# Kernel tuning notes

Measured on AMD Instinct MI355X. Metric: run time of the kernel, lower is better.

The kernel has to match this reference:

```python
import jax, jax.numpy as jnp
import numpy as np

B, L, E, H = 2, 2048, 1024, 16
HD = E // H  # 64
THETA = 10000.0


def setup_inputs() -> dict:
    key = jax.random.key(0)
    ks = jax.random.split(key, 9)
    s = 1.0 / np.sqrt(E)
    return {
        "x": jax.random.normal(ks[0], (B, L, E), jnp.float32),
        "Wq": jax.random.normal(ks[1], (E, E), jnp.float32) * s,
        "bq": jax.random.normal(ks[2], (E,), jnp.float32) * 0.01,
        "Wk": jax.random.normal(ks[3], (E, E), jnp.float32) * s,
        "bk": jax.random.normal(ks[4], (E,), jnp.float32) * 0.01,
        "Wv": jax.random.normal(ks[5], (E, E), jnp.float32) * s,
        "bv": jax.random.normal(ks[6], (E,), jnp.float32) * 0.01,
        "Wo": jax.random.normal(ks[7], (E, E), jnp.float32) * s,
        "bo": jax.random.normal(ks[8], (E,), jnp.float32) * 0.01,
    }


def _rope_tables(seq_len, dim, dtype):
    # lucidrains RotaryEmbedding: inv_freq over even indices, each freq repeated twice (interleaved)
    inv_freq = 1.0 / (THETA ** (jnp.arange(0, dim, 2, dtype=jnp.float32) / dim))
    freqs = jnp.arange(seq_len, dtype=jnp.float32)[:, None] * inv_freq[None, :]  # [L, dim/2]
    freqs = jnp.repeat(freqs, 2, axis=-1)  # [L, dim] -> f0,f0,f1,f1,...
    return jnp.cos(freqs).astype(dtype), jnp.sin(freqs).astype(dtype)


def _rotate_half(x):
    # interleaved pairs (x0, x1) -> (-x1, x0)
    x2 = x.reshape(*x.shape[:-1], -1, 2)
    x2 = jnp.stack([-x2[..., 1], x2[..., 0]], axis=-1)
    return x2.reshape(x.shape)


def _apply_rope(x, cos, sin):
    # x: [B, H, L, HD]; cos/sin: [L, HD]
    return x * cos[None, None] + _rotate_half(x) * sin[None, None]


def reference(x, Wq, bq, Wk, bk, Wv, bv, Wo, bo):
    b, l, e = x.shape
    q = (x @ Wq.T + bq).reshape(b, l, H, HD).transpose(0, 2, 1, 3)
    k = (x @ Wk.T + bk).reshape(b, l, H, HD).transpose(0, 2, 1, 3)
    v = (x @ Wv.T + bv).reshape(b, l, H, HD).transpose(0, 2, 1, 3)

    cos, sin = _rope_tables(l, HD, x.dtype)
    q = _apply_rope(q, cos, sin)
    k = _apply_rope(k, cos, sin)

    scale = 1.0 / np.sqrt(HD)
    scores = jnp.einsum("bhsd,bhed->bhse", q, k) * scale  # [B,H,L,L]
    attn = jax.nn.softmax(scores, axis=-1)
    out = jnp.einsum("bhse,bhed->bhsd", attn, v)  # [B,H,L,HD]
    out = out.transpose(0, 2, 1, 3).reshape(b, l, e)
    return out @ Wo.T + bo
```

## Files before the change

### kernel.cpp

```cpp
#include <hip/hip_runtime.h>

typedef unsigned short u16;
typedef __bf16 bf16x8 __attribute__((ext_vector_type(8)));
typedef float f32x4 __attribute__((ext_vector_type(4)));

#define LOG2E 1.4426950408889634f
#define EXP2(x) __builtin_amdgcn_exp2f(x)
#define NFM (-11.0f * LOG2E)

__device__ __forceinline__ u16 f2bf(float f) {
  unsigned int u = __float_as_uint(f);
  u += 0x7fffu + ((u >> 16) & 1u);
  return (u16)(u >> 16);
}

__device__ __forceinline__ void gld16(u16* lds, const u16* g) {
  __builtin_amdgcn_global_load_lds((const __attribute__((address_space(1))) unsigned int*)g,
                                   (__attribute__((address_space(3))) unsigned int*)lds,
                                   16, 0, 0);
}

__device__ __forceinline__ bf16x8 ldsv(const u16* p) {
  return *(const bf16x8*)p;
}

union U8 { uint4 u; bf16x8 v; };

__global__ __launch_bounds__(256) void k_prep(const float* __restrict__ x,
    const float* __restrict__ wq, const float* __restrict__ wk,
    const float* __restrict__ wv, const float* __restrict__ wo,
    u16* __restrict__ xb, u16* __restrict__ wqkvb, u16* __restrict__ wob,
    float* __restrict__ cosT, float* __restrict__ sinT) {
  unsigned gid = blockIdx.x * 256u + threadIdx.x;
  if (gid >= 2097152u) {
    unsigned t = gid - 2097152u;
    int l = t >> 5, i = t & 31;
    float inv = powf(10000.0f, -(float)i * (1.0f / 32.0f));
    float ang = (float)l * inv;
    float s, c;
    sincosf(ang, &s, &c);
    cosT[t] = c;
    sinT[t] = s;
    return;
  }
  const float4* src;
  u16* dst;
  unsigned off;
  if (gid < 1048576u)      { src = (const float4*)x;  dst = xb;              off = gid; }
  else if (gid < 1310720u) { src = (const float4*)wq; dst = wqkvb;           off = gid - 1048576u; }
  else if (gid < 1572864u) { src = (const float4*)wk; dst = wqkvb + 1048576; off = gid - 1310720u; }
  else if (gid < 1835008u) { src = (const float4*)wv; dst = wqkvb + 2097152; off = gid - 1572864u; }
  else                     { src = (const float4*)wo; dst = wob;             off = gid - 1835008u; }
  float4 f = src[off];
  ushort4 o;
  o.x = f2bf(f.x); o.y = f2bf(f.y); o.z = f2bf(f.z); o.w = f2bf(f.w);
  ((ushort4*)dst)[off] = o;
}

__device__ __forceinline__ void stage_tile(const u16* __restrict__ A, const u16* __restrict__ B,
                                           int m0, int n0, int kb, u16* dst) {
  const int tid = threadIdx.x;
#pragma unroll
  for (int it = 0; it < 4; ++it) {
    int idx = it * 256 + tid;
    int row = idx >> 3, c8 = idx & 7;
    int sc = c8 ^ (row & 7);
    gld16(dst + idx * 8,        A + (long)(m0 + row) * 1024 + kb + sc * 8);
    gld16(dst + 8192 + idx * 8, B + (long)(n0 + row) * 1024 + kb + sc * 8);
  }
}

__device__ __forceinline__ void gemm_loop(const u16* __restrict__ A, const u16* __restrict__ B,
                                          int m0, int n0, u16* S, f32x4 acc[4][4]) {
  const int tid = threadIdx.x;
  const int lane = tid & 63, wave = tid >> 6;
  const int quad = lane >> 4, l16 = lane & 15;
  const int wm = wave & 1, wn = wave >> 1;
  const int sw = l16 & 7;

#pragma unroll
  for (int i = 0; i < 4; ++i)
#pragma unroll
    for (int j = 0; j < 4; ++j)
      acc[i][j] = (f32x4){0.f, 0.f, 0.f, 0.f};

  stage_tile(A, B, m0, n0, 0, S);
  __syncthreads();

  for (int kt = 0; kt < 16; ++kt) {
    const int off = (kt & 1) << 14;
    const u16* As = S + off;
    const u16* Bs = S + off + 8192;
    if (kt < 15)
      stage_tile(A, B, m0, n0, (kt + 1) * 64, S + (off ^ 16384));
#pragma unroll
    for (int kk = 0; kk < 2; ++kk) {
      int ch = (kk * 4 + quad) ^ sw;
      bf16x8 a[4], b[4];
#pragma unroll
      for (int i = 0; i < 4; ++i)
        a[i] = ldsv(As + (wm * 64 + i * 16 + l16) * 64 + ch * 8);
#pragma unroll
      for (int j = 0; j < 4; ++j)
        b[j] = ldsv(Bs + (wn * 64 + j * 16 + l16) * 64 + ch * 8);
#pragma unroll
      for (int i = 0; i < 4; ++i)
#pragma unroll
        for (int j = 0; j < 4; ++j)
          acc[i][j] = __builtin_amdgcn_mfma_f32_16x16x32_bf16(a[i], b[j], acc[i][j], 0, 0, 0);
    }
    __syncthreads();
  }
}

__global__ __launch_bounds__(256) void k_qkv(const u16* __restrict__ xb, const u16* __restrict__ wqkvb,
    const float* __restrict__ bq, const float* __restrict__ bk, const float* __restrict__ bv,
    const float* __restrict__ cosT, const float* __restrict__ sinT,
    u16* __restrict__ Qg, u16* __restrict__ Kg, u16* __restrict__ VTg) {
  __shared__ __align__(16) u16 S[32768];
  f32x4 acc[4][4];
  int m0 = blockIdx.y * 128, n0 = blockIdx.x * 128;
  gemm_loop(xb, wqkvb, m0, n0, S, acc);

  const int tid = threadIdx.x, lane = tid & 63, wave = tid >> 6;
  const int quad = lane >> 4, l16 = lane & 15;
  const int wm = wave & 1, wn = wave >> 1;
  const int qsel = n0 >> 10;
  const int b = m0 >> 11;
  const int mb0 = m0 & 2047;

  if (qsel < 2) {
    const float* bp = qsel ? bk : bq;
#pragma unroll
    for (int j = 0; j < 4; ++j) {
      int nl = wn * 64 + j * 16 + l16;
      int n = n0 + nl;
      int fcol = n & 1023;
      int d = fcol & 63;
      int pi = d >> 1;
      float bias = bp[fcol];
      float sgn = (d & 1) ? 1.0f : -1.0f;
#pragma unroll
      for (int i = 0; i < 4; ++i) {
#pragma unroll
        for (int r = 0; r < 4; ++r) {
          int ml = wm * 64 + i * 16 + quad * 4 + r;
          int l = mb0 + ml;
          float v = acc[i][j][r] + bias;
          float partner = __shfl_xor(v, 1);
          float c = cosT[l * 32 + pi], s = sinT[l * 32 + pi];
          float o = fmaf(v, c, sgn * partner * s);
          if (qsel == 0) o *= 0.125f;
          S[ml * 132 + nl] = f2bf(o);
        }
      }
    }
    __syncthreads();
    u16* dstb = (qsel == 0) ? Qg : Kg;
#pragma unroll
    for (int t = 0; t < 16; ++t) {
      int idx = t * 256 + tid;
      int ml = idx >> 5, c4 = idx & 31;
      int n = n0 + c4 * 4;
      int h = (n & 1023) >> 6;
      int d = n & 63;
      *(uint2*)(dstb + (((long)b * 16 + h) * 2048 + mb0 + ml) * 64 + d) =
          *(const uint2*)(S + ml * 132 + c4 * 4);
    }
  } else {
#pragma unroll
    for (int j = 0; j < 4; ++j) {
      int nl = wn * 64 + j * 16 + l16;
      float bias = bv[(n0 + nl) & 1023];
#pragma unroll
      for (int i = 0; i < 4; ++i) {
        int mb = wm * 64 + i * 16 + quad * 4;
        unsigned u0 = (unsigned)f2bf(acc[i][j][0] + bias) | ((unsigned)f2bf(acc[i][j][1] + bias) << 16);
        unsigned u1 = (unsigned)f2bf(acc[i][j][2] + bias) | ((unsigned)f2bf(acc[i][j][3] + bias) << 16);
        *(uint2*)(S + nl * 132 + mb) = make_uint2(u0, u1);
      }
    }
    __syncthreads();
#pragma unroll
    for (int t = 0; t < 16; ++t) {
      int idx = t * 256 + tid;
      int nl = idx >> 5, c4 = idx & 31;
      int vcol = (n0 & 1023) + nl;
      int h = vcol >> 6, d = vcol & 63;
      *(uint2*)(VTg + (((long)b * 16 + h) * 64 + d) * 2048 + mb0 + c4 * 4) =
          *(const uint2*)(S + nl * 132 + c4 * 4);
    }
  }
}

__global__ __launch_bounds__(256, 2) void k_attn(const u16* __restrict__ Qg, const u16* __restrict__ Kg,
    const u16* __restrict__ VTg, u16* __restrict__ Ctx) {
  __shared__ __align__(16) char smem[34816];
  u16* Ks = (u16*)smem;
  u16* Vs = (u16*)(smem + 16384);
  const int tid = threadIdx.x, lane = tid & 63, wave = tid >> 6;
  const int quad = lane >> 4, l16 = lane & 15;
  const int wm = wave & 1, wsn = wave >> 1;
  const int sw = l16 & 7;
  const int bh = blockIdx.y;
  const int m0 = blockIdx.x * 128;
  const u16* Qb = Qg + (long)bh * 2048 * 64;
  const u16* Kb = Kg + (long)bh * 2048 * 64;
  const u16* Vb = VTg + (long)bh * 64 * 2048;

  bf16x8 qf[4][2];
#pragma unroll
  for (int mt = 0; mt < 4; ++mt)
#pragma unroll
    for (int kk = 0; kk < 2; ++kk)
      qf[mt][kk] = *(const bf16x8*)(Qb + (long)(m0 + wm * 64 + mt * 16 + l16) * 64 + kk * 32 + quad * 8);

  f32x4 oacc[4][4];
  float rs[4];
#pragma unroll
  for (int dt = 0; dt < 4; ++dt)
#pragma unroll
    for (int mt = 0; mt < 4; ++mt)
      oacc[dt][mt] = (f32x4){0.f, 0.f, 0.f, 0.f};
#pragma unroll
  for (int mt = 0; mt < 4; ++mt) rs[mt] = 0.f;

  for (int st = 0; st < 16; ++st) {
    int s0 = st * 128;
#pragma unroll
    for (int it = 0; it < 4; ++it) {
      int idx = it * 256 + tid;
      int row = idx >> 3, c8 = idx & 7;
      int sc = c8 ^ (row & 7);
      gld16(Ks + idx * 8, Kb + (long)(s0 + row) * 64 + sc * 8);
    }
#pragma unroll
    for (int it = 0; it < 4; ++it) {
      int idx = it * 256 + tid;
      int row = idx >> 4, g = idx & 15;
      uint4 vv = *(const uint4*)(Vb + (long)row * 2048 + s0 + g * 8);
      u16* wp = Vs + row * 132 + g * 8;
      *(uint2*)wp = make_uint2(vv.x, vv.y);
      *(uint2*)(wp + 4) = make_uint2(vv.z, vv.w);
    }
    __syncthreads();

    f32x4 sacc[4][4];
#pragma unroll
    for (int ct = 0; ct < 4; ++ct)
#pragma unroll
      for (int mt = 0; mt < 4; ++mt)
        sacc[ct][mt] = (f32x4){0.f, 0.f, 0.f, 0.f};
#pragma unroll
    for (int kk = 0; kk < 2; ++kk) {
      int ch = (kk * 4 + quad) ^ sw;
      bf16x8 kf[4];
#pragma unroll
      for (int ct = 0; ct < 4; ++ct)
        kf[ct] = ldsv(Ks + (wsn * 64 + ct * 16 + l16) * 64 + ch * 8);
#pragma unroll
      for (int ct = 0; ct < 4; ++ct)
#pragma unroll
        for (int mt = 0; mt < 4; ++mt)
          sacc[ct][mt] = __builtin_amdgcn_mfma_f32_16x16x32_bf16(kf[ct], qf[mt][kk], sacc[ct][mt], 0, 0, 0);
    }

#pragma unroll
    for (int c = 0; c < 2; ++c) {
      unsigned pk[2][4][2];
#pragma unroll
      for (int t = 0; t < 2; ++t) {
        int ct = c * 2 + t;
#pragma unroll
        for (int mt = 0; mt < 4; ++mt) {
          unsigned b[4];
          float sum = 0.f;
#pragma unroll
          for (int r = 0; r < 4; ++r) {
            float e = EXP2(fmaf(sacc[ct][mt][r], LOG2E, NFM));
            b[r] = __float_as_uint(e);
            sum += __uint_as_float(b[r] & 0xffff0000u);
          }
          rs[mt] += sum;
          pk[t][mt][0] = __builtin_amdgcn_perm(b[1], b[0], 0x07060302u);
          pk[t][mt][1] = __builtin_amdgcn_perm(b[3], b[2], 0x07060302u);
        }
      }
#pragma unroll
      for (int dt = 0; dt < 4; ++dt) {
        const u16* vp = Vs + (dt * 16 + l16) * 132 + wsn * 64 + c * 32 + quad * 4;
        uint2 lo = *(const uint2*)vp;
        uint2 hi = *(const uint2*)(vp + 16);
        U8 vfu; vfu.u = make_uint4(lo.x, lo.y, hi.x, hi.y);
#pragma unroll
        for (int mt = 0; mt < 4; ++mt) {
          U8 pfu; pfu.u = make_uint4(pk[0][mt][0], pk[0][mt][1], pk[1][mt][0], pk[1][mt][1]);
          oacc[dt][mt] = __builtin_amdgcn_mfma_f32_16x16x32_bf16(vfu.v, pfu.v, oacc[dt][mt], 0, 0, 0);
        }
      }
    }
    __syncthreads();
  }

  float* mbuf = (float*)smem;
  if (wsn == 1) {
#pragma unroll
    for (int dt = 0; dt < 4; ++dt)
#pragma unroll
      for (int mt = 0; mt < 4; ++mt)
#pragma unroll
        for (int r = 0; r < 4; ++r)
          mbuf[(wm * 68 + dt * 16 + mt * 4 + r) * 64 + lane] = oacc[dt][mt][r];
#pragma unroll
    for (int mt = 0; mt < 4; ++mt)
      mbuf[(wm * 68 + 64 + mt) * 64 + lane] = rs[mt];
  }
  __syncthreads();
  if (wsn == 0) {
#pragma unroll
    for (int dt = 0; dt < 4; ++dt)
#pragma unroll
      for (int mt = 0; mt < 4; ++mt)
#pragma unroll
        for (int r = 0; r < 4; ++r)
          oacc[dt][mt][r] += mbuf[(wm * 68 + dt * 16 + mt * 4 + r) * 64 + lane];
#pragma unroll
    for (int mt = 0; mt < 4; ++mt) {
      rs[mt] += mbuf[(wm * 68 + 64 + mt) * 64 + lane];
      rs[mt] += __shfl_xor(rs[mt], 16);
      rs[mt] += __shfl_xor(rs[mt], 32);
    }
    const int b = bh >> 4, h = bh & 15;
#pragma unroll
    for (int mt = 0; mt < 4; ++mt) {
      float inv = 1.0f / rs[mt];
      int tok = m0 + wm * 64 + mt * 16 + l16;
      u16* cp = Ctx + ((long)(b * 2048 + tok)) * 1024 + h * 64 + quad * 4;
#pragma unroll
      for (int dt = 0; dt < 4; ++dt) {
        float o0 = oacc[dt][mt][0] * inv, o1 = oacc[dt][mt][1] * inv;
        float o2 = oacc[dt][mt][2] * inv, o3 = oacc[dt][mt][3] * inv;
        unsigned u0 = (unsigned)f2bf(o0) | ((unsigned)f2bf(o1) << 16);
        unsigned u1 = (unsigned)f2bf(o2) | ((unsigned)f2bf(o3) << 16);
        *(uint2*)(cp + dt * 16) = make_uint2(u0, u1);
      }
    }
  }
}

__global__ __launch_bounds__(256) void k_out(const u16* __restrict__ Ctx, const u16* __restrict__ wob,
    const float* __restrict__ bo, float* __restrict__ out) {
  __shared__ __align__(16) u16 S[32768];
  f32x4 acc[4][4];
  int m0 = blockIdx.y * 128, n0 = blockIdx.x * 128;
  gemm_loop(Ctx, wob, m0, n0, S, acc);
  const int tid = threadIdx.x, lane = tid & 63, wave = tid >> 6;
  const int quad = lane >> 4, l16 = lane & 15;
  const int wm = wave & 1, wn = wave >> 1;
#pragma unroll
  for (int i = 0; i < 4; ++i)
#pragma unroll
    for (int j = 0; j < 4; ++j) {
      int n = n0 + wn * 64 + j * 16 + l16;
      float b_ = bo[n];
#pragma unroll
      for (int r = 0; r < 4; ++r) {
        int m = m0 + wm * 64 + i * 16 + quad * 4 + r;
        out[(long)m * 1024 + n] = acc[i][j][r] + b_;
      }
    }
}

extern "C" void kernel_launch(void* const* d_in, const int* in_sizes, int n_in,
                              void* d_out, int out_size, void* d_ws, size_t ws_size,
                              hipStream_t stream) {
  const float* x  = (const float*)d_in[0];
  const float* Wq = (const float*)d_in[1];
  const float* bq = (const float*)d_in[2];
  const float* Wk = (const float*)d_in[3];
  const float* bk = (const float*)d_in[4];
  const float* Wv = (const float*)d_in[5];
  const float* bv = (const float*)d_in[6];
  const float* Wo = (const float*)d_in[7];
  const float* bo = (const float*)d_in[8];
  float* out = (float*)d_out;

  char* ws = (char*)d_ws;
  u16* xb    = (u16*)(ws);
  u16* wqkvb = (u16*)(ws + (8ul << 20));
  u16* wob   = (u16*)(ws + (14ul << 20));
  u16* Qg    = (u16*)(ws + (16ul << 20));
  u16* Kg    = (u16*)(ws + (24ul << 20));
  u16* VTg   = (u16*)(ws + (32ul << 20));
  u16* Ctx   = (u16*)(ws + (40ul << 20));
  float* cosT = (float*)(ws + (48ul << 20));
  float* sinT = (float*)(ws + (48ul << 20) + (256ul << 10));

  k_prep<<<dim3(8448), dim3(256), 0, stream>>>(x, Wq, Wk, Wv, Wo, xb, wqkvb, wob, cosT, sinT);
  k_qkv<<<dim3(24, 32), dim3(256), 0, stream>>>(xb, wqkvb, bq, bk, bv, cosT, sinT, Qg, Kg, VTg);
  k_attn<<<dim3(16, 32), dim3(256), 0, stream>>>(Qg, Kg, VTg, Ctx);
  k_out<<<dim3(8, 32), dim3(256), 0, stream>>>(Ctx, wob, bo, out);
}
```

Measured before the change: 202.7 us.

## Double-buffer K tiles and register-prefetch V tiles in attention loop

Adds a second LDS buffer for K and issues the async global-to-LDS loads for the next K tile before computing on the current one. The next V tile is loaded into registers during compute and written to LDS after a barrier. This aims to hide global load latency behind the MFMA work. In exchange, LDS per block grows from about 34 KB to about 49 KB and register pressure rises, which may hurt occupancy at two blocks per CU.

```diff
diff --git a/kernel.cpp b/kernel.cpp
--- a/kernel.cpp
+++ b/kernel.cpp
@@ -195,9 +195,9 @@
 
 __global__ __launch_bounds__(256, 2) void k_attn(const u16* __restrict__ Qg, const u16* __restrict__ Kg,
     const u16* __restrict__ VTg, u16* __restrict__ Ctx) {
-  __shared__ __align__(16) char smem[34816];
+  __shared__ __align__(16) char smem[49664];
   u16* Ks = (u16*)smem;
-  u16* Vs = (u16*)(smem + 16384);
+  u16* Vs = (u16*)(smem + 32768);
   const int tid = threadIdx.x, lane = tid & 63, wave = tid >> 6;
   const int quad = lane >> 4, l16 = lane & 15;
   const int wm = wave & 1, wsn = wave >> 1;
@@ -225,25 +225,44 @@
 #pragma unroll
   for (int mt = 0; mt < 4; ++mt) rs[mt] = 0.f;
 
+#pragma unroll
+  for (int it = 0; it < 4; ++it) {
+    int idx = it * 256 + tid;
+    int row = idx >> 4, g = idx & 15;
+    uint4 vv = *(const uint4*)(Vb + (long)row * 2048 + g * 8);
+    u16* wp = Vs + row * 132 + g * 8;
+    *(uint2*)wp = make_uint2(vv.x, vv.y);
+    *(uint2*)(wp + 4) = make_uint2(vv.z, vv.w);
+  }
+#pragma unroll
+  for (int it = 0; it < 4; ++it) {
+    int idx = it * 256 + tid;
+    int row = idx >> 3, c8 = idx & 7;
+    int sc = c8 ^ (row & 7);
+    gld16(Ks + idx * 8, Kb + (long)row * 64 + sc * 8);
+  }
+  __syncthreads();
+
   for (int st = 0; st < 16; ++st) {
-    int s0 = st * 128;
-#pragma unroll
-    for (int it = 0; it < 4; ++it) {
-      int idx = it * 256 + tid;
-      int row = idx >> 3, c8 = idx & 7;
-      int sc = c8 ^ (row & 7);
-      gld16(Ks + idx * 8, Kb + (long)(s0 + row) * 64 + sc * 8);
-    }
-#pragma unroll
-    for (int it = 0; it < 4; ++it) {
-      int idx = it * 256 + tid;
-      int row = idx >> 4, g = idx & 15;
-      uint4 vv = *(const uint4*)(Vb + (long)row * 2048 + s0 + g * 8);
-      u16* wp = Vs + row * 132 + g * 8;
-      *(uint2*)wp = make_uint2(vv.x, vv.y);
-      *(uint2*)(wp + 4) = make_uint2(vv.z, vv.w);
-    }
-    __syncthreads();
+    const int cur = (st & 1) << 13;
+
+    uint4 vreg[4];
+    if (st < 15) {
+      int s0n = (st + 1) * 128;
+#pragma unroll
+      for (int it = 0; it < 4; ++it) {
+        int idx = it * 256 + tid;
+        int row = idx >> 4, g = idx & 15;
+        vreg[it] = *(const uint4*)(Vb + (long)row * 2048 + s0n + g * 8);
+      }
+#pragma unroll
+      for (int it = 0; it < 4; ++it) {
+        int idx = it * 256 + tid;
+        int row = idx >> 3, c8 = idx & 7;
+        int sc = c8 ^ (row & 7);
+        gld16(Ks + (cur ^ 8192) + idx * 8, Kb + (long)(s0n + row) * 64 + sc * 8);
+      }
+    }
 
     f32x4 sacc[4][4];
 #pragma unroll
@@ -257,7 +276,7 @@
       bf16x8 kf[4];
 #pragma unroll
       for (int ct = 0; ct < 4; ++ct)
-        kf[ct] = ldsv(Ks + (wsn * 64 + ct * 16 + l16) * 64 + ch * 8);
+        kf[ct] = ldsv(Ks + cur + (wsn * 64 + ct * 16 + l16) * 64 + ch * 8);
 #pragma unroll
       for (int ct = 0; ct < 4; ++ct)
 #pragma unroll
@@ -297,6 +316,18 @@
           U8 pfu; pfu.u = make_uint4(pk[0][mt][0], pk[0][mt][1], pk[1][mt][0], pk[1][mt][1]);
           oacc[dt][mt] = __builtin_amdgcn_mfma_f32_16x16x32_bf16(vfu.v, pfu.v, oacc[dt][mt], 0, 0, 0);
         }
+      }
+    }
+
+    __syncthreads();
+    if (st < 15) {
+#pragma unroll
+      for (int it = 0; it < 4; ++it) {
+        int idx = it * 256 + tid;
+        int row = idx >> 4, g = idx & 15;
+        u16* wp = Vs + row * 132 + g * 8;
+        *(uint2*)wp = make_uint2(vreg[it].x, vreg[it].y);
+        *(uint2*)(wp + 4) = make_uint2(vreg[it].z, vreg[it].w);
       }
     }
     __syncthreads();
```

After: 199.2 us. No clear change (-1.7%).
